# Kernel optimization log

Measured on AMD Instinct MI355X. Metric: run time of the kernel, lower is better.

The kernel has to match this reference:

```python
import jax, jax.numpy as jnp
import numpy as np

B, T, I, H = 256, 1024, 128, 256


def setup_inputs() -> dict:
    key = jax.random.key(0)
    ks = jax.random.split(key, 10)
    p = lambda k, shape: jax.random.normal(k, shape, dtype=jnp.float32) * 0.1
    return {
        "x": jax.random.normal(ks[0], (B, T, I), dtype=jnp.float32),
        # forget gate
        "f_wh": p(ks[1], (H, H)), "f_wx": p(ks[2], (I, H)), "f_b": p(ks[3], (H,)),
        # input (create) gate: potential (tanh) and percent (sigmoid) branches
        "i_wh_pot": p(ks[4], (H, H)), "i_wx_pot": p(ks[5], (I, H)), "i_b_pot": p(ks[6], (H,)),
        "i_wh_perc": p(ks[7], (H, H)), "i_wx_perc": p(ks[8], (I, H)), "i_b_perc": p(ks[9], (H,)),
        # output gate
        "o_wh": p(jax.random.fold_in(key, 10), (H, H)),
        "o_wx": p(jax.random.fold_in(key, 11), (I, H)),
        "o_b": p(jax.random.fold_in(key, 12), (H,)),
    }


def reference(x, f_wh, f_wx, f_b, i_wh_pot, i_wx_pot, i_b_pot,
              i_wh_perc, i_wx_perc, i_b_perc, o_wh, o_wx, o_b):
    # x: [B, T, I]
    sigmoid, tanh = jax.nn.sigmoid, jnp.tanh

    def step(carry, xt):  # xt: [B, I]
        s, l = carry  # short_term [B,H], long_term [B,H]
        forget = sigmoid(s @ f_wh + xt @ f_wx + f_b)
        create = sigmoid(s @ i_wh_perc + xt @ i_wx_perc + i_b_perc) * \
                 tanh(s @ i_wh_pot + xt @ i_wx_pot + i_b_pot)
        l_new = forget * l + create
        s_new = tanh(l_new) * sigmoid(s @ o_wh + xt @ o_wx + o_b)
        return (s_new, l_new), None

    init = (jnp.zeros((x.shape[0], f_b.shape[0]), x.dtype),
            jnp.zeros((x.shape[0], f_b.shape[0]), x.dtype))
    (short_term, long_term), _ = jax.lax.scan(step, init, jnp.swapaxes(x, 0, 1))
    return short_term, long_term
```

## Files before the change

### kernel.cpp

```cpp
#include <hip/hip_runtime.h>
#include <cstdint>

#define T_STEPS 1024
#define I_DIM 128
#define H_DIM 256

typedef __attribute__((ext_vector_type(8))) short bf16x8;
typedef __attribute__((ext_vector_type(4))) float f32x4;
typedef __attribute__((ext_vector_type(2))) unsigned int u32x2;

__device__ __forceinline__ uint32_t f2bf(float f) {
    uint32_t u = __builtin_bit_cast(uint32_t, f);
    return (u + 0x7FFFu + ((u >> 16) & 1u)) >> 16;
}
__device__ __forceinline__ uint32_t pk2bf(float lo, float hi) {
    return (f2bf(lo) & 0xFFFFu) | (f2bf(hi) << 16);
}
__device__ __forceinline__ float sigmoid_(float v) { return 1.f / (1.f + __expf(-v)); }
__device__ __forceinline__ float tanh_(float v) { float e = __expf(2.f * v); return 1.f - 2.f / (e + 1.f); }

__device__ __forceinline__ void barrier_lgkm() {
    asm volatile("s_waitcnt lgkmcnt(0)\n\ts_barrier" ::: "memory");
}

__global__ void __launch_bounds__(256, 1)
lstm_kernel(const float* __restrict__ x,
            const float* __restrict__ f_wh, const float* __restrict__ f_wx, const float* __restrict__ f_b,
            const float* __restrict__ p_wh, const float* __restrict__ p_wx, const float* __restrict__ p_b,
            const float* __restrict__ c_wh, const float* __restrict__ c_wx, const float* __restrict__ c_b,
            const float* __restrict__ o_wh, const float* __restrict__ o_wx, const float* __restrict__ o_b,
            float* __restrict__ out, uint8_t* __restrict__ ws)
{
    __shared__ __align__(16) uint8_t lds[65792];
    uint8_t* WH = lds;
    uint8_t* WX = lds + 32768;
    uint8_t* SL = lds + 49152;
    uint8_t* XT = lds + 57344;
    float*   GB = (float*)(lds + 61440);

    const int tid  = (int)threadIdx.x;
    const int lane = tid & 63;
    const int wv   = tid >> 6;
    const int blk  = (int)blockIdx.x;
    const int grp  = blk & 15;
    const int cwg  = blk >> 4;
    const int grow0 = grp << 4;
    const int hc0   = cwg << 4;

    uint8_t* FAST = ws + 4096;
    uint8_t* MIRR = ws + 4096 + 524288;

    const float* wh = (wv == 0) ? f_wh : (wv == 1) ? p_wh : (wv == 2) ? c_wh : o_wh;
    const float* wx = (wv == 0) ? f_wx : (wv == 1) ? p_wx : (wv == 2) ? c_wx : o_wx;
    const float* bp = (wv == 0) ? f_b  : (wv == 1) ? p_b  : (wv == 2) ? c_b  : o_b;

    {
        const int col = lane & 15, kc = lane >> 4;
        const uint32_t csw = (uint32_t)((col & 7) << 4);
        uint8_t* whb = WH + (size_t)(wv * 16 + col) * 512;
        #pragma unroll
        for (int it = 0; it < 8; ++it) {
            const int k0 = it * 32 + kc * 8;
            float v0 = wh[(size_t)(k0 + 0) * H_DIM + hc0 + col];
            float v1 = wh[(size_t)(k0 + 1) * H_DIM + hc0 + col];
            float v2 = wh[(size_t)(k0 + 2) * H_DIM + hc0 + col];
            float v3 = wh[(size_t)(k0 + 3) * H_DIM + hc0 + col];
            float v4 = wh[(size_t)(k0 + 4) * H_DIM + hc0 + col];
            float v5 = wh[(size_t)(k0 + 5) * H_DIM + hc0 + col];
            float v6 = wh[(size_t)(k0 + 6) * H_DIM + hc0 + col];
            float v7 = wh[(size_t)(k0 + 7) * H_DIM + hc0 + col];
            uint4 pk;
            pk.x = pk2bf(v0, v1); pk.y = pk2bf(v2, v3);
            pk.z = pk2bf(v4, v5); pk.w = pk2bf(v6, v7);
            *(uint4*)(whb + (((uint32_t)(it * 64 + kc * 16)) ^ csw)) = pk;
        }
        uint8_t* wxb = WX + (size_t)(wv * 16 + col) * 256;
        #pragma unroll
        for (int it = 0; it < 4; ++it) {
            const int k0 = it * 32 + kc * 8;
            float v0 = wx[(size_t)(k0 + 0) * H_DIM + hc0 + col];
            float v1 = wx[(size_t)(k0 + 1) * H_DIM + hc0 + col];
            float v2 = wx[(size_t)(k0 + 2) * H_DIM + hc0 + col];
            float v3 = wx[(size_t)(k0 + 3) * H_DIM + hc0 + col];
            float v4 = wx[(size_t)(k0 + 4) * H_DIM + hc0 + col];
            float v5 = wx[(size_t)(k0 + 5) * H_DIM + hc0 + col];
            float v6 = wx[(size_t)(k0 + 6) * H_DIM + hc0 + col];
            float v7 = wx[(size_t)(k0 + 7) * H_DIM + hc0 + col];
            uint4 pk;
            pk.x = pk2bf(v0, v1); pk.y = pk2bf(v2, v3);
            pk.z = pk2bf(v4, v5); pk.w = pk2bf(v6, v7);
            *(uint4*)(wxb + (((uint32_t)(it * 64 + kc * 16)) ^ csw)) = pk;
        }
    }
    const float bias = bp[hc0 + (lane & 15)];
    __syncthreads();

    const int fr = lane & 15, fkc = lane >> 4;
    const uint32_t fsw = (uint32_t)((fr & 7) << 4);
    uint8_t* slA = SL + (size_t)fr * 512;
    uint8_t* xtA = XT + (size_t)fr * 256;
    const uint8_t* whB = WH + (size_t)(wv * 16 + fr) * 512;
    const uint8_t* wxB = WX + (size_t)(wv * 16 + fr) * 256;

    uint4 bwh[8], bwx[4];
    #pragma unroll
    for (int q = 0; q < 8; ++q)
        bwh[q] = *(const uint4*)(whB + (((uint32_t)(q * 64 + fkc * 16)) ^ fsw));
    #pragma unroll
    for (int q = 0; q < 4; ++q)
        bwx[q] = *(const uint4*)(wxB + (((uint32_t)(q * 64 + fkc * 16)) ^ fsw));

    const int crow = tid >> 4, ccol = tid & 15;
    const size_t pub_off = (size_t)(grow0 + crow) * 1024 + (size_t)(cwg * 8 + (ccol >> 1)) * 8;

    if ((tid & 1) == 0) {
        u32x2 pd; pd.x = 0u; pd.y = 1u;
        asm volatile("global_store_dwordx2 %0, %1, off" :: "v"(FAST + pub_off), "v"(pd) : "memory");
        asm volatile("global_store_dwordx2 %0, %1, off sc0 sc1" :: "v"(MIRR + pub_off), "v"(pd) : "memory");
    }

    const int xrow = tid >> 4, xseg = tid & 15;
    const uint32_t xsw = (uint32_t)((xrow & 7) << 4);
    const float* xptr = x + (size_t)(grow0 + xrow) * (T_STEPS * I_DIM) + xseg * 8;
    float4 xr0 = *(const float4*)(xptr);
    float4 xr1 = *(const float4*)(xptr + 4);

    const size_t poll_off = (size_t)(grow0 + xrow) * 1024 + (size_t)xseg * 64;

    bool slow = false;
    float l_reg = 0.f, s_fin = 0.f, l_fin = 0.f;

    for (int t = 0; t < T_STEPS; ++t) {
        {
            uint4 pk;
            pk.x = pk2bf(xr0.x, xr0.y); pk.y = pk2bf(xr0.z, xr0.w);
            pk.z = pk2bf(xr1.x, xr1.y); pk.w = pk2bf(xr1.z, xr1.w);
            *(uint4*)(XT + (size_t)xrow * 256 + (((uint32_t)(xseg * 16)) ^ xsw)) = pk;
        }
        {
            const int tn = (t + 1 < T_STEPS) ? (t + 1) : (T_STEPS - 1);
            const float* p = xptr + (size_t)tn * I_DIM;
            xr0 = *(const float4*)(p);
            xr1 = *(const float4*)(p + 4);
        }
        barrier_lgkm();

        f32x4 accA = {0.f, 0.f, 0.f, 0.f};
        #pragma unroll
        for (int q = 0; q < 4; ++q) {
            uint4 av = *(const uint4*)(xtA + (((uint32_t)(q * 64 + fkc * 16)) ^ fsw));
            accA = __builtin_amdgcn_mfma_f32_16x16x32_bf16(
                __builtin_bit_cast(bf16x8, av), __builtin_bit_cast(bf16x8, bwx[q]), accA, 0, 0, 0);
        }

        uint4 g0, g1, g2, g3;
        uint32_t m = 1u;
        const uint32_t e = (uint32_t)t + 1u;
        const size_t par = (size_t)((t & 1) ? 262144 : 0);
        if (!slow) {
            const uint8_t* src = FAST + par + poll_off;
            const int budget = (t == 0) ? 1024 : 64;
            int rounds = 0;
            do {
                asm volatile("global_load_dwordx4 %0, %1, off sc0"
                             : "=v"(g0) : "v"(src) : "memory");
                asm volatile("global_load_dwordx4 %0, %1, off offset:16 sc0"
                             : "=v"(g1) : "v"(src) : "memory");
                asm volatile("global_load_dwordx4 %0, %1, off offset:32 sc0"
                             : "=v"(g2) : "v"(src) : "memory");
                asm volatile("global_load_dwordx4 %0, %1, off offset:48 sc0"
                             : "=v"(g3) : "v"(src) : "memory");
                asm volatile("s_waitcnt vmcnt(0)" ::: "memory");
                __builtin_amdgcn_sched_barrier(0);
                m = (g0.y ^ e) | (g0.w ^ e) | (g1.y ^ e) | (g1.w ^ e)
                  | (g2.y ^ e) | (g2.w ^ e) | (g3.y ^ e) | (g3.w ^ e);
                if (m == 0) break;
            } while (++rounds < budget);
            if (m != 0) slow = true;
        }
        if (m != 0) {
            const uint8_t* src = MIRR + par + poll_off;
            do {
                asm volatile("global_load_dwordx4 %0, %1, off sc0 sc1"
                             : "=v"(g0) : "v"(src) : "memory");
                asm volatile("global_load_dwordx4 %0, %1, off offset:16 sc0 sc1"
                             : "=v"(g1) : "v"(src) : "memory");
                asm volatile("global_load_dwordx4 %0, %1, off offset:32 sc0 sc1"
                             : "=v"(g2) : "v"(src) : "memory");
                asm volatile("global_load_dwordx4 %0, %1, off offset:48 sc0 sc1"
                             : "=v"(g3) : "v"(src) : "memory");
                asm volatile("s_waitcnt vmcnt(0)" ::: "memory");
                __builtin_amdgcn_sched_barrier(0);
                m = (g0.y ^ e) | (g0.w ^ e) | (g1.y ^ e) | (g1.w ^ e)
                  | (g2.y ^ e) | (g2.w ^ e) | (g3.y ^ e) | (g3.w ^ e);
            } while (m != 0);
        }

        {
            uint4 d0; d0.x = g0.x; d0.y = g0.z; d0.z = g1.x; d0.w = g1.z;
            uint4 d1; d1.x = g2.x; d1.y = g2.z; d1.z = g3.x; d1.w = g3.z;
            uint8_t* dst = SL + (size_t)xrow * 512;
            const uint32_t o = (uint32_t)(xseg * 32);
            *(uint4*)(dst + (o ^ xsw)) = d0;
            *(uint4*)(dst + ((o + 16) ^ xsw)) = d1;
        }
        barrier_lgkm();

        f32x4 accB = {0.f, 0.f, 0.f, 0.f};
        #pragma unroll
        for (int q = 0; q < 4; ++q) {
            uint4 a0 = *(const uint4*)(slA + (((uint32_t)(q * 64 + fkc * 16)) ^ fsw));
            uint4 a1 = *(const uint4*)(slA + (((uint32_t)((q + 4) * 64 + fkc * 16)) ^ fsw));
            accA = __builtin_amdgcn_mfma_f32_16x16x32_bf16(
                __builtin_bit_cast(bf16x8, a0), __builtin_bit_cast(bf16x8, bwh[q]), accA, 0, 0, 0);
            accB = __builtin_amdgcn_mfma_f32_16x16x32_bf16(
                __builtin_bit_cast(bf16x8, a1), __builtin_bit_cast(bf16x8, bwh[q + 4]), accB, 0, 0, 0);
        }

        #pragma unroll
        for (int j = 0; j < 4; ++j) {
            const float pre = accA[j] + accB[j] + bias;
            const float a = (wv == 1) ? tanh_(pre) : sigmoid_(pre);
            GB[wv * 272 + (fkc * 4 + j) * 17 + fr] = a;
        }
        barrier_lgkm();

        {
            const float fg  = GB[0 * 272 + crow * 17 + ccol];
            const float pot = GB[1 * 272 + crow * 17 + ccol];
            const float prc = GB[2 * 272 + crow * 17 + ccol];
            const float og  = GB[3 * 272 + crow * 17 + ccol];
            const float lnew = fg * l_reg + prc * pot;
            const float snew = tanh_(lnew) * og;
            l_reg = lnew;
            if (t == T_STEPS - 1) { s_fin = snew; l_fin = lnew; }
            const uint32_t sb = f2bf(snew);
            const uint32_t ob = (uint32_t)__shfl_xor((int)sb, 1, 64);
            if (((tid & 1) == 0) && (t != T_STEPS - 1)) {
                const size_t po = (size_t)(((t + 1) & 1) ? 262144 : 0) + pub_off;
                u32x2 pd; pd.x = (sb & 0xFFFFu) | (ob << 16); pd.y = (uint32_t)t + 2u;
                asm volatile("global_store_dwordx2 %0, %1, off" :: "v"(FAST + po), "v"(pd) : "memory");
                asm volatile("global_store_dwordx2 %0, %1, off sc0 sc1" :: "v"(MIRR + po), "v"(pd) : "memory");
            }
        }
    }

    out[(size_t)(grow0 + crow) * H_DIM + hc0 + ccol] = s_fin;
    out[(size_t)H_DIM * H_DIM + (size_t)(grow0 + crow) * H_DIM + hc0 + ccol] = l_fin;
}

extern "C" void kernel_launch(void* const* d_in, const int* in_sizes, int n_in,
                              void* d_out, int out_size, void* d_ws, size_t ws_size,
                              hipStream_t stream) {
    const float* x    = (const float*)d_in[0];
    const float* f_wh = (const float*)d_in[1];
    const float* f_wx = (const float*)d_in[2];
    const float* f_b  = (const float*)d_in[3];
    const float* p_wh = (const float*)d_in[4];
    const float* p_wx = (const float*)d_in[5];
    const float* p_b  = (const float*)d_in[6];
    const float* c_wh = (const float*)d_in[7];
    const float* c_wx = (const float*)d_in[8];
    const float* c_b  = (const float*)d_in[9];
    const float* o_wh = (const float*)d_in[10];
    const float* o_wx = (const float*)d_in[11];
    const float* o_b  = (const float*)d_in[12];
    float* outp = (float*)d_out;
    uint8_t* wsp = (uint8_t*)d_ws;

    hipMemsetAsync(d_ws, 0, 4096 + 2 * 524288, stream);

    void* args[] = { (void*)&x,
                     (void*)&f_wh, (void*)&f_wx, (void*)&f_b,
                     (void*)&p_wh, (void*)&p_wx, (void*)&p_b,
                     (void*)&c_wh, (void*)&c_wx, (void*)&c_b,
                     (void*)&o_wh, (void*)&o_wx, (void*)&o_b,
                     (void*)&outp, (void*)&wsp };
    hipLaunchCooperativeKernel((const void*)lstm_kernel, dim3(256), dim3(256), args, 0, stream);
}
```

Before: 2.431 ms.

## Issue state gather loads early and remap block-to-group/column indexing

New measurement: 2.990 ms. 23.0% more time.

```diff
diff --git a/kernel.cpp b/kernel.cpp
--- a/kernel.cpp
+++ b/kernel.cpp
@@ -22,6 +22,15 @@
 __device__ __forceinline__ void barrier_lgkm() {
     asm volatile("s_waitcnt lgkmcnt(0)\n\ts_barrier" ::: "memory");
 }
+
+#define ISSUE_GATHER(PTR, SCB)                                                          \
+    asm volatile("global_load_dwordx4 %0, %1, off " SCB : "=v"(g0) : "v"(PTR) : "memory"); \
+    asm volatile("global_load_dwordx4 %0, %1, off offset:16 " SCB : "=v"(g1) : "v"(PTR) : "memory"); \
+    asm volatile("global_load_dwordx4 %0, %1, off offset:32 " SCB : "=v"(g2) : "v"(PTR) : "memory"); \
+    asm volatile("global_load_dwordx4 %0, %1, off offset:48 " SCB : "=v"(g3) : "v"(PTR) : "memory");
+
+#define TAGMASK() ((g0.y ^ e) | (g0.w ^ e) | (g1.y ^ e) | (g1.w ^ e) \
+                 | (g2.y ^ e) | (g2.w ^ e) | (g3.y ^ e) | (g3.w ^ e))
 
 __global__ void __launch_bounds__(256, 1)
 lstm_kernel(const float* __restrict__ x,
@@ -42,8 +51,8 @@
     const int lane = tid & 63;
     const int wv   = tid >> 6;
     const int blk  = (int)blockIdx.x;
-    const int grp  = blk & 15;
-    const int cwg  = blk >> 4;
+    const int grp  = blk >> 4;
+    const int cwg  = blk & 15;
     const int grow0 = grp << 4;
     const int hc0   = cwg << 4;
 
@@ -131,6 +140,15 @@
     float l_reg = 0.f, s_fin = 0.f, l_fin = 0.f;
 
     for (int t = 0; t < T_STEPS; ++t) {
+        const uint32_t e = (uint32_t)t + 1u;
+        const size_t par = (size_t)((t & 1) ? 262144 : 0);
+        const uint8_t* fsrc = FAST + par + poll_off;
+        const uint8_t* msrc = MIRR + par + poll_off;
+
+        uint4 g0, g1, g2, g3;
+        if (!slow) { ISSUE_GATHER(fsrc, "sc0") }
+        else       { ISSUE_GATHER(msrc, "sc0 sc1") }
+
         {
             uint4 pk;
             pk.x = pk2bf(xr0.x, xr0.y); pk.y = pk2bf(xr0.z, xr0.w);
@@ -153,47 +171,28 @@
                 __builtin_bit_cast(bf16x8, av), __builtin_bit_cast(bf16x8, bwx[q]), accA, 0, 0, 0);
         }
 
-        uint4 g0, g1, g2, g3;
-        uint32_t m = 1u;
-        const uint32_t e = (uint32_t)t + 1u;
-        const size_t par = (size_t)((t & 1) ? 262144 : 0);
-        if (!slow) {
-            const uint8_t* src = FAST + par + poll_off;
-            const int budget = (t == 0) ? 1024 : 64;
-            int rounds = 0;
-            do {
-                asm volatile("global_load_dwordx4 %0, %1, off sc0"
-                             : "=v"(g0) : "v"(src) : "memory");
-                asm volatile("global_load_dwordx4 %0, %1, off offset:16 sc0"
-                             : "=v"(g1) : "v"(src) : "memory");
-                asm volatile("global_load_dwordx4 %0, %1, off offset:32 sc0"
-                             : "=v"(g2) : "v"(src) : "memory");
-                asm volatile("global_load_dwordx4 %0, %1, off offset:48 sc0"
-                             : "=v"(g3) : "v"(src) : "memory");
+        asm volatile("s_waitcnt vmcnt(0)" ::: "memory");
+        __builtin_amdgcn_sched_barrier(0);
+        uint32_t m = TAGMASK();
+        if (m != 0) {
+            if (!slow) {
+                const int budget = (t == 0) ? 1024 : 64;
+                int rounds = 0;
+                do {
+                    ISSUE_GATHER(fsrc, "sc0")
+                    asm volatile("s_waitcnt vmcnt(0)" ::: "memory");
+                    __builtin_amdgcn_sched_barrier(0);
+                    m = TAGMASK();
+                    if (m == 0) break;
+                } while (++rounds < budget);
+                if (m != 0) slow = true;
+            }
+            while (m != 0) {
+                ISSUE_GATHER(msrc, "sc0 sc1")
                 asm volatile("s_waitcnt vmcnt(0)" ::: "memory");
                 __builtin_amdgcn_sched_barrier(0);
-                m = (g0.y ^ e) | (g0.w ^ e) | (g1.y ^ e) | (g1.w ^ e)
-                  | (g2.y ^ e) | (g2.w ^ e) | (g3.y ^ e) | (g3.w ^ e);
-                if (m == 0) break;
-            } while (++rounds < budget);
-            if (m != 0) slow = true;
-        }
-        if (m != 0) {
-            const uint8_t* src = MIRR + par + poll_off;
-            do {
-                asm volatile("global_load_dwordx4 %0, %1, off sc0 sc1"
-                             : "=v"(g0) : "v"(src) : "memory");
-                asm volatile("global_load_dwordx4 %0, %1, off offset:16 sc0 sc1"
-                             : "=v"(g1) : "v"(src) : "memory");
-                asm volatile("global_load_dwordx4 %0, %1, off offset:32 sc0 sc1"
-                             : "=v"(g2) : "v"(src) : "memory");
-                asm volatile("global_load_dwordx4 %0, %1, off offset:48 sc0 sc1"
-                             : "=v"(g3) : "v"(src) : "memory");
-                asm volatile("s_waitcnt vmcnt(0)" ::: "memory");
-                __builtin_amdgcn_sched_barrier(0);
-                m = (g0.y ^ e) | (g0.w ^ e) | (g1.y ^ e) | (g1.w ^ e)
-                  | (g2.y ^ e) | (g2.w ^ e) | (g3.y ^ e) | (g3.w ^ e);
-            } while (m != 0);
+                m = TAGMASK();
+            }
         }
 
         {
```
